# Performance work log

Hardware: AMD Instinct MI355X
Metric: run time of the kernel (lower is better)

Reference implementation:

```python
import jax, jax.numpy as jnp
import numpy as np
import math

H = 5120        # hidden_size
NH = 32         # num heads
HD = H // NH    # head_dim = 160
B = 1
S = 2048
TRAIN_SEQLEN = 8192
BASE = 10000.0


def _rotary_cos_sin(seq_len):
    # Eval-mode RotaryEmbedding: seq_len clamped to training_seqlen, NTK alpha + mscale (logN) scaling.
    eff = max(seq_len, TRAIN_SEQLEN)
    scale = eff / TRAIN_SEQLEN
    mscale = 1.0 if scale <= 1.0 else 0.1 * math.log(scale) + 1.0
    ntk_alpha = max(2 ** math.ceil(math.log(eff / 4096, 2) + 1) - 1, 1)
    base = BASE * ntk_alpha ** (HD / (HD - 2))
    inv_freq = 1.0 / base ** (np.arange(0, HD, 2, dtype=np.float64) / HD)
    t = np.arange(eff, dtype=np.float64)
    freqs = np.outer(t, inv_freq)              # [eff, HD/2]
    emb = np.concatenate([freqs, freqs], axis=-1)  # [eff, HD]
    cos = (mscale * np.cos(emb))[:seq_len].astype(np.float32)
    sin = (mscale * np.sin(emb))[:seq_len].astype(np.float32)
    return jnp.asarray(cos), jnp.asarray(sin)


def _rotate_half(x):
    x1, x2 = x[..., : HD // 2], x[..., HD // 2 :]
    return jnp.concatenate([-x2, x1], axis=-1)


def setup_inputs() -> dict:
    key = jax.random.key(0)
    ks = jax.random.split(key, 6)
    hidden_states = jax.random.normal(ks[0], (B, S, H), jnp.float32)
    residual = jax.random.normal(ks[1], (B, S, H), jnp.float32)
    # boolean causal mask, True = masked (matches masked_fill semantics)
    attention_mask = jnp.triu(jnp.ones((S, S), dtype=bool), k=1)[None, None]
    Wq = jax.random.normal(ks[2], (H, H), jnp.float32) * 0.02      # query: Linear(h, h, bias=False)
    Wkv = jax.random.normal(ks[3], (2 * H, H), jnp.float32) * 0.02  # key_value: Linear(h, 2h, bias=False)
    Wd = jax.random.normal(ks[4], (H, H), jnp.float32) * 0.02       # dense: Linear(h, h) with bias
    bd = jnp.zeros((H,), jnp.float32)
    return {
        "hidden_states": hidden_states,
        "residual": residual,
        "attention_mask": attention_mask,
        "Wq": Wq,
        "Wkv": Wkv,
        "Wd": Wd,
        "bd": bd,
    }


def reference(hidden_states, residual, attention_mask, Wq, Wkv, Wd, bd):
    b, s, h = hidden_states.shape
    # QKV projections (torch Linear: y = x @ W.T)
    q = jnp.einsum('bsh,oh->bso', hidden_states, Wq).reshape(b, s, NH, HD)
    kv = jnp.einsum('bsh,oh->bso', hidden_states, Wkv).reshape(b, s, NH, 2 * HD)
    k, v = kv[..., :HD], kv[..., HD:]
    # rotary embedding with logN mscale folded into cos/sin
    cos, sin = _rotary_cos_sin(s)               # [s, HD]
    cos = cos[None, :, None, :]
    sin = sin[None, :, None, :]
    q = q * cos + _rotate_half(q) * sin
    k = k * cos + _rotate_half(k) * sin
    inv_norm = 1.0 / math.sqrt(HD)
    scores = jnp.einsum('bqnd,bknd->bnqk', q, k) * inv_norm   # [b, nh, s, s]
    scores = jnp.where(attention_mask, jnp.finfo(scores.dtype).min, scores)
    probs = jax.nn.softmax(scores, axis=-1)
    # attention_dropout p=0.0 -> identity
    ctx = jnp.einsum('bnqk,bknd->bqnd', probs, v).reshape(b, s, h)
    out = ctx @ Wd.T + bd
    # dropout_add with hidden_dropout=0.0 (eval) -> residual + out
    return residual + out
```

## Files before the change

### kernel.cpp

```cpp
#include <hip/hip_runtime.h>
#include <cmath>

typedef unsigned short u16;
typedef unsigned int   u32;

using bf16x8 = __attribute__((ext_vector_type(8))) short;
using f32x4  = __attribute__((ext_vector_type(4))) float;

#define S_LEN 2048
#define NHEAD 32
#define HDIM  160
#define HID   5120

__device__ __forceinline__ f32x4 mfma16(bf16x8 a, bf16x8 b, f32x4 c) {
  return __builtin_amdgcn_mfma_f32_16x16x32_bf16(a, b, c, 0, 0, 0);
}

__device__ __forceinline__ u16 f2bf(float f) {
  u32 u = __builtin_bit_cast(u32, f);
  u += 0x7FFFu + ((u >> 16) & 1u);
  return (u16)(u >> 16);
}
__device__ __forceinline__ float bf2f(u16 h) {
  u32 u = ((u32)h) << 16;
  return __builtin_bit_cast(float, u);
}

__device__ __forceinline__ void gload16(const void* g, void* l) {
  __builtin_amdgcn_global_load_lds((const __attribute__((address_space(1))) void*)g,
                                   (__attribute__((address_space(3))) void*)l, 16, 0, 0);
}

__global__ void cvt_bf16_kernel(const float* __restrict__ in, u16* __restrict__ out, int n8) {
  int i = blockIdx.x * 256 + threadIdx.x;
  if (i >= n8) return;
  const float4* p = (const float4*)in + (size_t)i * 2;
  float4 a = p[0], b = p[1];
  uint4 o;
  o.x = (u32)f2bf(a.x) | ((u32)f2bf(a.y) << 16);
  o.y = (u32)f2bf(a.z) | ((u32)f2bf(a.w) << 16);
  o.z = (u32)f2bf(b.x) | ((u32)f2bf(b.y) << 16);
  o.w = (u32)f2bf(b.z) | ((u32)f2bf(b.w) << 16);
  ((uint4*)out)[i] = o;
}

__global__ void rope_table_kernel(float2* __restrict__ tab) {
  int i = blockIdx.x * 256 + threadIdx.x;
  if (i >= S_LEN * 80) return;
  int s = i / 80, j = i % 80;
  double base = 10000.0 * pow(3.0, 160.0 / 158.0);
  double invf = pow(base, -((double)(2 * j)) / 160.0);
  double ang  = fmod((double)s * invf, 6.283185307179586476925287);
  tab[i] = make_float2((float)cos(ang), (float)sin(ang));
}

__global__ void rope_apply_kernel(const u16* __restrict__ src, const float2* __restrict__ tab,
                                  u16* __restrict__ dst, int headStride, int rowStride) {
  int i = blockIdx.x * 256 + threadIdx.x;
  if (i >= S_LEN * NHEAD * 80) return;
  int dp = i % 80; int sh = i / 80; int h = sh % NHEAD; int s = sh / NHEAD;
  int d = 2 * dp;
  const u16* row = src + (size_t)s * rowStride + h * headStride;
  u32 q01 = *(const u32*)&row[d];
  u32 p01 = *(const u32*)&row[d < 80 ? d + 80 : d - 80];
  int j = (d < 80) ? d : d - 80;
  float2 cs0 = tab[s * 80 + j];
  float2 cs1 = tab[s * 80 + j + 1];
  float q0 = bf2f((u16)(q01 & 0xffff)), q1 = bf2f((u16)(q01 >> 16));
  float p0 = bf2f((u16)(p01 & 0xffff)), p1 = bf2f((u16)(p01 >> 16));
  float sgn = (d < 80) ? -1.f : 1.f;
  float o0 = q0 * cs0.x + sgn * p0 * cs0.y;
  float o1 = q1 * cs1.x + sgn * p1 * cs1.y;
  u32 o = (u32)f2bf(o0) | ((u32)f2bf(o1) << 16);
  *(u32*)&dst[((size_t)h * S_LEN + s) * HDIM + d] = o;
}

__global__ void vtrans_kernel(const u16* __restrict__ KV, u16* __restrict__ Vt) {
  __shared__ u16 T[HDIM][72];
  int h = blockIdx.y; int s0 = blockIdx.x * 64; int tid = threadIdx.x;
  for (int i = tid; i < 64 * 80; i += 256) {
    int s = i / 80, dp = i % 80;
    u32 v = *(const u32*)&KV[(size_t)(s0 + s) * (2 * HID) + h * 320 + 160 + 2 * dp];
    T[2 * dp][s]     = (u16)(v & 0xffff);
    T[2 * dp + 1][s] = (u16)(v >> 16);
  }
  __syncthreads();
  for (int i = tid; i < HDIM * 32; i += 256) {
    int d = i / 32, sp = i % 32;
    u32 v = (u32)T[d][2 * sp] | ((u32)T[d][2 * sp + 1] << 16);
    *(u32*)&Vt[((size_t)h * HDIM + d) * S_LEN + s0 + 2 * sp] = v;
  }
}

template<int EPI>
__global__ __launch_bounds__(256, 2) void gemm_bt(
    const u16* __restrict__ A, const u16* __restrict__ Bm, void* __restrict__ Cout,
    int M, int N, int K, const float* __restrict__ bias, const float* __restrict__ resid)
{
  int tid = threadIdx.x;
  int wv = tid >> 6, l = tid & 63, l15 = l & 15, l4 = l >> 4;
  int bm = blockIdx.y * 128, bn = blockIdx.x * 128;
  __shared__ u16 As[128 * 32], Bs[128 * 32];
  f32x4 acc[4][4];
#pragma unroll
  for (int i = 0; i < 4; i++)
#pragma unroll
    for (int j = 0; j < 4; j++) acc[i][j] = f32x4{0.f, 0.f, 0.f, 0.f};

  int wm = (wv >> 1) * 64, wn = (wv & 1) * 64;
  const u16* gA = A + (size_t)(bm + (tid >> 2)) * K + (tid & 3) * 8;
  const u16* gB = Bm + (size_t)(bn + (tid >> 2)) * K + (tid & 3) * 8;
  u16* ldsA = As + wv * 16 * 32;
  u16* ldsB = Bs + wv * 16 * 32;

  for (int k0 = 0; k0 < K; k0 += 32) {
    __syncthreads();
    gload16(gA + k0, ldsA);
    gload16(gA + (size_t)64 * K + k0, ldsA + 64 * 32);
    gload16(gB + k0, ldsB);
    gload16(gB + (size_t)64 * K + k0, ldsB + 64 * 32);
    __syncthreads();
    bf16x8 af[4], bfr[4];
#pragma unroll
    for (int i = 0; i < 4; i++) af[i] = *(const bf16x8*)&As[(wm + i * 16 + l15) * 32 + l4 * 8];
#pragma unroll
    for (int i = 0; i < 4; i++) bfr[i] = *(const bf16x8*)&Bs[(wn + i * 16 + l15) * 32 + l4 * 8];
#pragma unroll
    for (int mi = 0; mi < 4; mi++)
#pragma unroll
      for (int ni = 0; ni < 4; ni++) acc[mi][ni] = mfma16(af[mi], bfr[ni], acc[mi][ni]);
  }

#pragma unroll
  for (int mi = 0; mi < 4; mi++)
#pragma unroll
    for (int ni = 0; ni < 4; ni++) {
      int row0 = bm + wm + mi * 16 + l4 * 4;
      int col  = bn + wn + ni * 16 + l15;
      if (EPI == 0) {
        u16* C = (u16*)Cout;
#pragma unroll
        for (int r = 0; r < 4; r++) C[(size_t)(row0 + r) * N + col] = f2bf(acc[mi][ni][r]);
      } else {
        float* C = (float*)Cout;
        float b = bias[col];
#pragma unroll
        for (int r = 0; r < 4; r++) {
          size_t idx = (size_t)(row0 + r) * N + col;
          C[idx] = acc[mi][ni][r] + b + resid[idx];
        }
      }
    }
}

__global__ __launch_bounds__(512, 4) void attn_kernel(
    const u16* __restrict__ Qr, const u16* __restrict__ Kr,
    const u16* __restrict__ Vt, u16* __restrict__ ctx)
{
  int lin = blockIdx.x;
  int qx = 15 - (lin >> 5);
  int h  = lin & 31;
  int q0 = qx * 128;
  int tid = threadIdx.x;
  int w = tid >> 6, l = tid & 63, l15 = l & 15, l4 = l >> 4;
  int qb = q0 + w * 16;

  __shared__ u16 Ks[64][164];
  __shared__ u16 Vs[160][68];
  __shared__ u16 Plds[8][16][68];

  const u16* Qh = Qr + (size_t)h * S_LEN * HDIM;
  const u16* Kh = Kr + (size_t)h * S_LEN * HDIM;
  const u16* Vh = Vt + (size_t)h * HDIM * S_LEN;

  bf16x8 aQ[5];
#pragma unroll
  for (int kc = 0; kc < 5; kc++)
    aQ[kc] = *(const bf16x8*)&Qh[(size_t)(qb + l15) * HDIM + kc * 32 + l4 * 8];

  f32x4 accO[10];
#pragma unroll
  for (int dt = 0; dt < 10; dt++) accO[dt] = f32x4{0.f, 0.f, 0.f, 0.f};
  float mrun[4], lrun[4];
#pragma unroll
  for (int r = 0; r < 4; r++) { mrun[r] = -1e30f; lrun[r] = 0.f; }

  const float c2 = 0.07905694150420949f * 1.44269504088896f;
  int Tend = 2 * qx + 2;

  {
    uint4 rg[5];
#pragma unroll
    for (int i = 0; i < 5; i++) {
      int u = tid + 512 * i;
      if (u < 1280) { int row = u / 20, c = u % 20;
        rg[i] = *(const uint4*)&Kh[(size_t)row * HDIM + c * 8]; }
      else { int v = u - 1280; int row = v >> 3, c = v & 7;
        rg[i] = *(const uint4*)&Vh[(size_t)row * S_LEN + c * 8]; }
    }
#pragma unroll
    for (int i = 0; i < 5; i++) {
      int u = tid + 512 * i;
      if (u < 1280) { int row = u / 20, c = u % 20; *(uint4*)&Ks[row][c * 8] = rg[i]; }
      else { int v = u - 1280; int row = v >> 3, c = v & 7; *(uint4*)&Vs[row][c * 8] = rg[i]; }
    }
  }
  __syncthreads();

  for (int t = 0; t < Tend; ++t) {
    int k0 = t * 64;
    bool more = (t + 1 < Tend);
    uint4 rg[5];
    if (more) {
      int k1 = k0 + 64;
#pragma unroll
      for (int i = 0; i < 5; i++) {
        int u = tid + 512 * i;
        if (u < 1280) { int row = u / 20, c = u % 20;
          rg[i] = *(const uint4*)&Kh[(size_t)(k1 + row) * HDIM + c * 8]; }
        else { int v = u - 1280; int row = v >> 3, c = v & 7;
          rg[i] = *(const uint4*)&Vh[(size_t)row * S_LEN + k1 + c * 8]; }
      }
    }

    if (k0 <= qb + 15) {
      f32x4 s_[4];
#pragma unroll
      for (int nt = 0; nt < 4; nt++) s_[nt] = f32x4{0.f, 0.f, 0.f, 0.f};

#pragma unroll
      for (int kc = 0; kc < 5; kc++) {
        bf16x8 bK[4];
#pragma unroll
        for (int nt = 0; nt < 4; nt++)
          bK[nt] = *(const bf16x8*)&Ks[nt * 16 + l15][kc * 32 + l4 * 8];
#pragma unroll
        for (int nt = 0; nt < 4; nt++) s_[nt] = mfma16(aQ[kc], bK[nt], s_[nt]);
      }

      if (k0 + 63 > qb) {
#pragma unroll
        for (int nt = 0; nt < 4; nt++)
#pragma unroll
          for (int r = 0; r < 4; r++) {
            int kk = k0 + nt * 16 + l15;
            int qq = qb + l4 * 4 + r;
            if (kk > qq) s_[nt][r] = -1e30f;
          }
      }

      float sf[4];
#pragma unroll
      for (int r = 0; r < 4; r++) {
        float v = fmaxf(fmaxf(s_[0][r], s_[1][r]), fmaxf(s_[2][r], s_[3][r]));
#pragma unroll
        for (int m = 1; m <= 8; m <<= 1) v = fmaxf(v, __shfl_xor(v, m));
        float mnew = fmaxf(mrun[r], v);
        sf[r] = exp2f((mrun[r] - mnew) * c2);
        mrun[r] = mnew;
      }
      float rsum[4] = {0.f, 0.f, 0.f, 0.f};
#pragma unroll
      for (int nt = 0; nt < 4; nt++)
#pragma unroll
        for (int r = 0; r < 4; r++) {
          float p = exp2f((s_[nt][r] - mrun[r]) * c2);
          s_[nt][r] = p;
          rsum[r] += p;
        }
#pragma unroll
      for (int r = 0; r < 4; r++) {
        float v = rsum[r];
#pragma unroll
        for (int m = 1; m <= 8; m <<= 1) v += __shfl_xor(v, m);
        lrun[r] = lrun[r] * sf[r] + v;
      }
#pragma unroll
      for (int dt = 0; dt < 10; dt++)
#pragma unroll
        for (int r = 0; r < 4; r++) accO[dt][r] *= sf[r];
#pragma unroll
      for (int nt = 0; nt < 4; nt++)
#pragma unroll
        for (int r = 0; r < 4; r++)
          Plds[w][l4 * 4 + r][nt * 16 + l15] = f2bf(s_[nt][r]);

#pragma unroll
      for (int kc = 0; kc < 2; kc++) {
        bf16x8 aP = *(const bf16x8*)&Plds[w][l15][kc * 32 + l4 * 8];
        bf16x8 bV[10];
#pragma unroll
        for (int dt = 0; dt < 10; dt++)
          bV[dt] = *(const bf16x8*)&Vs[dt * 16 + l15][kc * 32 + l4 * 8];
#pragma unroll
        for (int dt = 0; dt < 10; dt++)
          accO[dt] = mfma16(aP, bV[dt], accO[dt]);
      }
    }

    __syncthreads();
    if (more) {
#pragma unroll
      for (int i = 0; i < 5; i++) {
        int u = tid + 512 * i;
        if (u < 1280) { int row = u / 20, c = u % 20; *(uint4*)&Ks[row][c * 8] = rg[i]; }
        else { int v = u - 1280; int row = v >> 3, c = v & 7; *(uint4*)&Vs[row][c * 8] = rg[i]; }
      }
    }
    __syncthreads();
  }

  float inv[4];
#pragma unroll
  for (int r = 0; r < 4; r++) inv[r] = 1.0f / lrun[r];
#pragma unroll
  for (int dt = 0; dt < 10; dt++)
#pragma unroll
    for (int r = 0; r < 4; r++) {
      int q = qb + l4 * 4 + r;
      ctx[(size_t)q * HID + h * HDIM + dt * 16 + l15] = f2bf(accO[dt][r] * inv[r]);
    }
}

extern "C" void kernel_launch(void* const* d_in, const int* in_sizes, int n_in,
                              void* d_out, int out_size, void* d_ws, size_t ws_size,
                              hipStream_t stream) {
  const float* hs    = (const float*)d_in[0];
  const float* resid = (const float*)d_in[1];
  const float* Wq  = (const float*)d_in[3];
  const float* Wkv = (const float*)d_in[4];
  const float* Wd  = (const float*)d_in[5];
  const float* bd  = (const float*)d_in[6];
  float* out = (float*)d_out;

  char* ws = (char*)d_ws;
  const size_t SH  = (size_t)S_LEN * HID;
  u16* Xb    = (u16*)(ws);                        size_t off = SH * 2;
  u16* Wqb   = (u16*)(ws + off);                  off += (size_t)HID * HID * 2;
  u16* Wkvb  = (u16*)(ws + off);                  off += (size_t)2 * HID * HID * 2;
  u16* Wdb   = (u16*)(ws + off);                  off += (size_t)HID * HID * 2;
  u16* Qraw  = (u16*)(ws + off);                  off += SH * 2;
  u16* KVraw = (u16*)(ws + off);                  off += SH * 2 * 2;
  u16* Qr    = (u16*)(ws + off);                  off += SH * 2;
  u16* Kr    = (u16*)(ws + off);                  off += SH * 2;
  u16* Vt    = (u16*)(ws + off);                  off += SH * 2;
  u16* ctx   = (u16*)(ws + off);                  off += SH * 2;
  float2* tab = (float2*)(ws + off);              off += (size_t)S_LEN * 80 * 8;

  cvt_bf16_kernel<<<(int)(SH / 8 / 256), 256, 0, stream>>>(hs, Xb, (int)(SH / 8));
  cvt_bf16_kernel<<<HID * HID / 8 / 256, 256, 0, stream>>>(Wq, Wqb, HID * HID / 8);
  cvt_bf16_kernel<<<2 * HID * HID / 8 / 256, 256, 0, stream>>>(Wkv, Wkvb, 2 * HID * HID / 8);
  cvt_bf16_kernel<<<HID * HID / 8 / 256, 256, 0, stream>>>(Wd, Wdb, HID * HID / 8);

  rope_table_kernel<<<(S_LEN * 80 + 255) / 256, 256, 0, stream>>>(tab);

  gemm_bt<0><<<dim3(HID / 128, S_LEN / 128), 256, 0, stream>>>(Xb, Wqb, Qraw, S_LEN, HID, HID, nullptr, nullptr);
  gemm_bt<0><<<dim3(2 * HID / 128, S_LEN / 128), 256, 0, stream>>>(Xb, Wkvb, KVraw, S_LEN, 2 * HID, HID, nullptr, nullptr);

  rope_apply_kernel<<<S_LEN * NHEAD * 80 / 256, 256, 0, stream>>>(Qraw, tab, Qr, HDIM, HID);
  rope_apply_kernel<<<S_LEN * NHEAD * 80 / 256, 256, 0, stream>>>(KVraw, tab, Kr, 2 * HDIM, 2 * HID);
  vtrans_kernel<<<dim3(S_LEN / 64, NHEAD), 256, 0, stream>>>(KVraw, Vt);

  attn_kernel<<<512, 512, 0, stream>>>(Qr, Kr, Vt, ctx);

  gemm_bt<1><<<dim3(HID / 128, S_LEN / 128), 256, 0, stream>>>(ctx, Wdb, out, S_LEN, HID, HID, bd, resid);
}
```

Baseline: 996.4 us.

## Replace GEMM with 256x256 double-buffered tiled kernel and fuse QKV projections

Replaces the 128x128 single-buffered GEMM with a 256x256-tile, 512-thread kernel. It uses double-buffered LDS with async global-to-LDS loads, an XOR-swizzled LDS layout, block index swizzling for L2 locality, and s_setprio around the MFMA bursts. The Q and KV weight matrices are packed contiguously so a single GEMM produces a fused QKV buffer, and the rope and vtrans kernels read from it with the new stride. This is meant to cut global/LDS traffic per flop and overlap loads with compute, in exchange for heavier register use (128 accumulators per thread) and fewer workgroups (the dense GEMM gets only 160 blocks).

```diff
diff --git a/kernel.cpp b/kernel.cpp
--- a/kernel.cpp
+++ b/kernel.cpp
@@ -11,6 +11,7 @@
 #define NHEAD 32
 #define HDIM  160
 #define HID   5120
+#define NQKV  15360
 
 __device__ __forceinline__ f32x4 mfma16(bf16x8 a, bf16x8 b, f32x4 c) {
   return __builtin_amdgcn_mfma_f32_16x16x32_bf16(a, b, c, 0, 0, 0);
@@ -75,12 +76,12 @@
   *(u32*)&dst[((size_t)h * S_LEN + s) * HDIM + d] = o;
 }
 
-__global__ void vtrans_kernel(const u16* __restrict__ KV, u16* __restrict__ Vt) {
+__global__ void vtrans_kernel(const u16* __restrict__ src, u16* __restrict__ Vt, int rowStride) {
   __shared__ u16 T[HDIM][72];
   int h = blockIdx.y; int s0 = blockIdx.x * 64; int tid = threadIdx.x;
   for (int i = tid; i < 64 * 80; i += 256) {
     int s = i / 80, dp = i % 80;
-    u32 v = *(const u32*)&KV[(size_t)(s0 + s) * (2 * HID) + h * 320 + 160 + 2 * dp];
+    u32 v = *(const u32*)&src[(size_t)(s0 + s) * rowStride + h * 320 + 2 * dp];
     T[2 * dp][s]     = (u16)(v & 0xffff);
     T[2 * dp + 1][s] = (u16)(v >> 16);
   }
@@ -93,50 +94,101 @@
 }
 
 template<int EPI>
-__global__ __launch_bounds__(256, 2) void gemm_bt(
+__global__ __launch_bounds__(512, 2) void gemm256(
     const u16* __restrict__ A, const u16* __restrict__ Bm, void* __restrict__ Cout,
     int M, int N, int K, const float* __restrict__ bias, const float* __restrict__ resid)
 {
+  __shared__ u16 As[2][2][8192];
+  __shared__ u16 Bs[2][2][8192];
   int tid = threadIdx.x;
-  int wv = tid >> 6, l = tid & 63, l15 = l & 15, l4 = l >> 4;
-  int bm = blockIdx.y * 128, bn = blockIdx.x * 128;
-  __shared__ u16 As[128 * 32], Bs[128 * 32];
-  f32x4 acc[4][4];
-#pragma unroll
-  for (int i = 0; i < 4; i++)
+  int w = tid >> 6, l = tid & 63, l15 = l & 15, l4 = l >> 4;
+  int wr = w >> 2, wc = w & 3;
+
+  int nbx = gridDim.x;
+  int nwg = nbx * gridDim.y;
+  int lin = blockIdx.y * nbx + blockIdx.x;
+  int cpx = nwg >> 3;
+  int swz = (lin & 7) * cpx + (lin >> 3);
+  int bm = (swz / nbx) * 256, bn = (swz % nbx) * 256;
+
+  int srow = tid >> 2;
+  int scol = ((tid & 3) * 8) ^ ((srow & 8) ? 16 : 0);
+  const u16* gA0 = A  + (size_t)(bm +       srow) * K + scol;
+  const u16* gA1 = A  + (size_t)(bm + 128 + srow) * K + scol;
+  const u16* gB0 = Bm + (size_t)(bn +       srow) * K + scol;
+  const u16* gB1 = Bm + (size_t)(bn + 128 + srow) * K + scol;
+  int dstoff = w * 512;
+
+  f32x4 acc[8][4];
+#pragma unroll
+  for (int i = 0; i < 8; i++)
 #pragma unroll
     for (int j = 0; j < 4; j++) acc[i][j] = f32x4{0.f, 0.f, 0.f, 0.f};
 
-  int wm = (wv >> 1) * 64, wn = (wv & 1) * 64;
-  const u16* gA = A + (size_t)(bm + (tid >> 2)) * K + (tid & 3) * 8;
-  const u16* gB = Bm + (size_t)(bn + (tid >> 2)) * K + (tid & 3) * 8;
-  u16* ldsA = As + wv * 16 * 32;
-  u16* ldsB = Bs + wv * 16 * 32;
-
-  for (int k0 = 0; k0 < K; k0 += 32) {
-    __syncthreads();
-    gload16(gA + k0, ldsA);
-    gload16(gA + (size_t)64 * K + k0, ldsA + 64 * 32);
-    gload16(gB + k0, ldsB);
-    gload16(gB + (size_t)64 * K + k0, ldsB + 64 * 32);
-    __syncthreads();
-    bf16x8 af[4], bfr[4];
-#pragma unroll
-    for (int i = 0; i < 4; i++) af[i] = *(const bf16x8*)&As[(wm + i * 16 + l15) * 32 + l4 * 8];
-#pragma unroll
-    for (int i = 0; i < 4; i++) bfr[i] = *(const bf16x8*)&Bs[(wn + i * 16 + l15) * 32 + l4 * 8];
-#pragma unroll
-    for (int mi = 0; mi < 4; mi++)
-#pragma unroll
-      for (int ni = 0; ni < 4; ni++) acc[mi][ni] = mfma16(af[mi], bfr[ni], acc[mi][ni]);
+  int cA = (l4 * 8) ^ ((l15 & 8) ? 16 : 0);
+  const int NT = K >> 6;
+
+  auto STAGE = [&](int kt, int p) {
+    int k0 = kt << 6;
+    gload16(gA0 + k0,      &As[p][0][dstoff]);
+    gload16(gA0 + k0 + 32, &As[p][0][4096 + dstoff]);
+    gload16(gA1 + k0,      &As[p][1][dstoff]);
+    gload16(gA1 + k0 + 32, &As[p][1][4096 + dstoff]);
+    gload16(gB0 + k0,      &Bs[p][0][dstoff]);
+    gload16(gB0 + k0 + 32, &Bs[p][0][4096 + dstoff]);
+    gload16(gB1 + k0,      &Bs[p][1][dstoff]);
+    gload16(gB1 + k0 + 32, &Bs[p][1][4096 + dstoff]);
+  };
+
+  STAGE(0, 0);
+  for (int kt = 0; kt < NT; ++kt) {
+    int p = kt & 1;
+    if (kt + 1 < NT) {
+      STAGE(kt + 1, p ^ 1);
+      asm volatile("s_waitcnt vmcnt(8)" ::: "memory");
+    } else {
+      asm volatile("s_waitcnt vmcnt(0)" ::: "memory");
+    }
+    __builtin_amdgcn_s_barrier();
+
+    const u16* Ah = &As[p][wr][0];
+    const u16* Bh = &Bs[p][wc >> 1][0];
+    int bcol = (wc & 1) * 64;
+#pragma unroll
+    for (int q = 0; q < 4; ++q) {
+      int qm = q >> 1, qn = q & 1;
+      bf16x8 aF[4][2], bF[2][2];
+#pragma unroll
+      for (int mi = 0; mi < 4; ++mi)
+#pragma unroll
+        for (int kk = 0; kk < 2; ++kk)
+          aF[mi][kk] = *(const bf16x8*)&Ah[kk * 4096 + (qm * 64 + mi * 16 + l15) * 32 + cA];
+#pragma unroll
+      for (int ni = 0; ni < 2; ++ni)
+#pragma unroll
+        for (int kk = 0; kk < 2; ++kk)
+          bF[ni][kk] = *(const bf16x8*)&Bh[kk * 4096 + (bcol + qn * 32 + ni * 16 + l15) * 32 + cA];
+      __builtin_amdgcn_s_barrier();
+      __builtin_amdgcn_s_setprio(1);
+#pragma unroll
+      for (int kk = 0; kk < 2; ++kk)
+#pragma unroll
+        for (int mi = 0; mi < 4; ++mi)
+#pragma unroll
+          for (int ni = 0; ni < 2; ++ni)
+            acc[qm * 4 + mi][qn * 2 + ni] =
+                mfma16(aF[mi][kk], bF[ni][kk], acc[qm * 4 + mi][qn * 2 + ni]);
+      __builtin_amdgcn_s_setprio(0);
+      __builtin_amdgcn_s_barrier();
+    }
   }
 
 #pragma unroll
-  for (int mi = 0; mi < 4; mi++)
-#pragma unroll
-    for (int ni = 0; ni < 4; ni++) {
-      int row0 = bm + wm + mi * 16 + l4 * 4;
-      int col  = bn + wn + ni * 16 + l15;
+  for (int mi = 0; mi < 8; ++mi)
+#pragma unroll
+    for (int ni = 0; ni < 4; ++ni) {
+      int row0 = bm + wr * 128 + mi * 16 + l4 * 4;
+      int col  = bn + wc * 64 + ni * 16 + l15;
       if (EPI == 0) {
         u16* C = (u16*)Cout;
 #pragma unroll
@@ -334,34 +386,33 @@
   float* out = (float*)d_out;
 
   char* ws = (char*)d_ws;
-  const size_t SH  = (size_t)S_LEN * HID;
-  u16* Xb    = (u16*)(ws);                        size_t off = SH * 2;
-  u16* Wqb   = (u16*)(ws + off);                  off += (size_t)HID * HID * 2;
-  u16* Wkvb  = (u16*)(ws + off);                  off += (size_t)2 * HID * HID * 2;
-  u16* Wdb   = (u16*)(ws + off);                  off += (size_t)HID * HID * 2;
-  u16* Qraw  = (u16*)(ws + off);                  off += SH * 2;
-  u16* KVraw = (u16*)(ws + off);                  off += SH * 2 * 2;
-  u16* Qr    = (u16*)(ws + off);                  off += SH * 2;
-  u16* Kr    = (u16*)(ws + off);                  off += SH * 2;
-  u16* Vt    = (u16*)(ws + off);                  off += SH * 2;
-  u16* ctx   = (u16*)(ws + off);                  off += SH * 2;
-  float2* tab = (float2*)(ws + off);              off += (size_t)S_LEN * 80 * 8;
+  const size_t SH = (size_t)S_LEN * HID;
+  u16* Xb     = (u16*)(ws);                        size_t off = SH * 2;
+  u16* Wqkvb  = (u16*)(ws + off);                  off += (size_t)3 * HID * HID * 2;
+  u16* Wdb    = (u16*)(ws + off);                  off += (size_t)HID * HID * 2;
+  u16* QKVraw = (u16*)(ws + off);                  off += (size_t)S_LEN * NQKV * 2;
+  u16* Qr     = (u16*)(ws + off);                  off += SH * 2;
+  u16* Kr     = (u16*)(ws + off);                  off += SH * 2;
+  u16* Vt     = (u16*)(ws + off);                  off += SH * 2;
+  u16* ctx    = (u16*)(ws + off);                  off += SH * 2;
+  float2* tab = (float2*)(ws + off);               off += (size_t)S_LEN * 80 * 8;
 
   cvt_bf16_kernel<<<(int)(SH / 8 / 256), 256, 0, stream>>>(hs, Xb, (int)(SH / 8));
-  cvt_bf16_kernel<<<HID * HID / 8 / 256, 256, 0, stream>>>(Wq, Wqb, HID * HID / 8);
-  cvt_bf16_kernel<<<2 * HID * HID / 8 / 256, 256, 0, stream>>>(Wkv, Wkvb, 2 * HID * HID / 8);
+  cvt_bf16_kernel<<<HID * HID / 8 / 256, 256, 0, stream>>>(Wq, Wqkvb, HID * HID / 8);
+  cvt_bf16_kernel<<<2 * HID * HID / 8 / 256, 256, 0, stream>>>(Wkv, Wqkvb + (size_t)HID * HID, 2 * HID * HID / 8);
   cvt_bf16_kernel<<<HID * HID / 8 / 256, 256, 0, stream>>>(Wd, Wdb, HID * HID / 8);
 
   rope_table_kernel<<<(S_LEN * 80 + 255) / 256, 256, 0, stream>>>(tab);
 
-  gemm_bt<0><<<dim3(HID / 128, S_LEN / 128), 256, 0, stream>>>(Xb, Wqb, Qraw, S_LEN, HID, HID, nullptr, nullptr);
-  gemm_bt<0><<<dim3(2 * HID / 128, S_LEN / 128), 256, 0, stream>>>(Xb, Wkvb, KVraw, S_LEN, 2 * HID, HID, nullptr, nullptr);
-
-  rope_apply_kernel<<<S_LEN * NHEAD * 80 / 256, 256, 0, stream>>>(Qraw, tab, Qr, HDIM, HID);
-  rope_apply_kernel<<<S_LEN * NHEAD * 80 / 256, 256, 0, stream>>>(KVraw, tab, Kr, 2 * HDIM, 2 * HID);
-  vtrans_kernel<<<dim3(S_LEN / 64, NHEAD), 256, 0, stream>>>(KVraw, Vt);
+  gemm256<0><<<dim3(NQKV / 256, S_LEN / 256), 512, 0, stream>>>(
+      Xb, Wqkvb, QKVraw, S_LEN, NQKV, HID, nullptr, nullptr);
+
+  rope_apply_kernel<<<S_LEN * NHEAD * 80 / 256, 256, 0, stream>>>(QKVraw, tab, Qr, HDIM, NQKV);
+  rope_apply_kernel<<<S_LEN * NHEAD * 80 / 256, 256, 0, stream>>>(QKVraw + HID, tab, Kr, 2 * HDIM, NQKV);
+  vtrans_kernel<<<dim3(S_LEN / 64, NHEAD), 256, 0, stream>>>(QKVraw + HID + HDIM, Vt, NQKV);
 
   attn_kernel<<<512, 512, 0, stream>>>(Qr, Kr, Vt, ctx);
 
-  gemm_bt<1><<<dim3(HID / 128, S_LEN / 128), 256, 0, stream>>>(ctx, Wdb, out, S_LEN, HID, HID, bd, resid);
-}
+  gemm256<1><<<dim3(HID / 256, S_LEN / 256), 512, 0, stream>>>(
+      ctx, Wdb, out, S_LEN, HID, HID, bd, resid);
+}
```

After: 1.194 ms. 19.8% more time.
